# Kernel optimization log

Hardware: AMD Instinct MI355X
Metric: run time of the kernel (lower is better)

The kernel has to match this reference:

```python
import jax, jax.numpy as jnp
import numpy as np

K = 3  # kernel_size from init_kwargs


def setup_inputs() -> dict:
    key = jax.random.key(0)
    x = jax.random.normal(key, (32, 64, 56, 56), dtype=jnp.float32)
    return {"x": x}


def reference(x):
    # Faithful translation of Shift.forward: for each channel i, for each
    # (dy, dx) in the kernel window, emit the padded slice
    # x_pad[:, i, dy:dy+h, dx:dx+w]. Concatenation order is channel-major,
    # then row-major over (dy, dx), which equals stacking the k*k shifts on
    # a new axis right after the channel axis and flattening.
    n, c, h, w = x.shape
    pad = K // 2
    xp = jnp.pad(x, ((0, 0), (0, 0), (pad, pad), (pad, pad)))
    # k*k shifted views of shape [n, c, h, w]; loop is over a small fixed
    # offset set (9 for k=3), not over data dims.
    shifts = jnp.stack(
        [xp[:, :, dy:dy + h, dx:dx + w] for dy in range(K) for dx in range(K)],
        axis=2,
    )  # [n, c, k*k, h, w]
    return shifts.reshape(n, c * K * K, h, w)
```

## Files before the change

kernel.cpp:

```cpp
#include <hip/hip_runtime.h>


#define N_ 32
#define C_ 64
#define H_ 56
#define W_ 56
#define W4 14
#define PLANE (H_ * W_)
#define POS_PER_PLANE (H_ * W4)
#define TOTAL (N_ * C_ * POS_PER_PLANE)

typedef float f4 __attribute__((ext_vector_type(4)));

__global__ __launch_bounds__(256) void shift_kernel(const float* __restrict__ x,
                                                    float* __restrict__ out) {
    int t = blockIdx.x * blockDim.x + threadIdx.x;
    if (t >= TOTAL) return;

    int w4 = t % W4;
    int r  = t / W4;
    int h  = r % H_;
    int nc = r / H_;

    int w0 = w4 * 4;
    const float* plane = x + (long)nc * PLANE;

    float rowbuf[3][6];
#pragma unroll
    for (int d = 0; d < 3; ++d) {
        int ih = h + d - 1;
        if (ih < 0 || ih >= H_) {
#pragma unroll
            for (int j = 0; j < 6; ++j) rowbuf[d][j] = 0.f;
        } else {
            const float* rp = plane + ih * W_;
            f4 v = *(const f4*)(rp + w0);
            rowbuf[d][1] = v.x;
            rowbuf[d][2] = v.y;
            rowbuf[d][3] = v.z;
            rowbuf[d][4] = v.w;
            rowbuf[d][0] = (w4 > 0)      ? rp[w0 - 1] : 0.f;
            rowbuf[d][5] = (w4 < W4 - 1) ? rp[w0 + 4] : 0.f;
        }
    }

    float* ob = out + ((long)(nc * 9) * H_ + h) * W_ + w0;
#pragma unroll
    for (int dy = 0; dy < 3; ++dy) {
#pragma unroll
        for (int dx = 0; dx < 3; ++dx) {
            f4 v = { rowbuf[dy][dx],     rowbuf[dy][dx + 1],
                     rowbuf[dy][dx + 2], rowbuf[dy][dx + 3] };
            *(f4*)(ob + (long)(dy * 3 + dx) * PLANE) = v;
        }
    }
}

extern "C" void kernel_launch(void* const* d_in, const int* in_sizes, int n_in,
                              void* d_out, int out_size, void* d_ws, size_t ws_size,
                              hipStream_t stream) {
    const float* x = (const float*)d_in[0];
    float* out = (float*)d_out;

    int block = 256;
    int grid = (TOTAL + block - 1) / block;
    shift_kernel<<<grid, block, 0, stream>>>(x, out);
}
```

Before: 245.7 us.

## Stage each channel plane in LDS with zero halo and stream shifted outputs

Each block now handles one (n,c) plane. It loads the plane into a zero-padded LDS tile, then writes all nine shifted output planes from LDS using nontemporal vector stores. This replaces redundant, partly unaligned global reads and per-element boundary branches with LDS reads. In exchange it adds two block barriers, an LDS zero-fill pass and unaligned LDS reads, and launches only 2048 blocks.

```diff
diff --git a/kernel.cpp b/kernel.cpp
--- a/kernel.cpp
+++ b/kernel.cpp
@@ -7,51 +7,43 @@
 #define W_ 56
 #define W4 14
 #define PLANE (H_ * W_)
-#define POS_PER_PLANE (H_ * W4)
-#define TOTAL (N_ * C_ * POS_PER_PLANE)
+#define PLANE4 (H_ * W4)
+#define LROW 68
+#define LROWS 58
+#define LSIZE (LROWS * LROW)
 
 typedef float f4 __attribute__((ext_vector_type(4)));
 
 __global__ __launch_bounds__(256) void shift_kernel(const float* __restrict__ x,
-                                                    float* __restrict__ out) {
-    int t = blockIdx.x * blockDim.x + threadIdx.x;
-    if (t >= TOTAL) return;
+                                                    f4* __restrict__ out) {
+    __shared__ float lds[LSIZE];
+    const int tid = threadIdx.x;
+    const int nc  = blockIdx.x;
 
-    int w4 = t % W4;
-    int r  = t / W4;
-    int h  = r % H_;
-    int nc = r / H_;
+    for (int i = tid; i < LSIZE; i += 256) lds[i] = 0.f;
+    __syncthreads();
 
-    int w0 = w4 * 4;
-    const float* plane = x + (long)nc * PLANE;
+    const f4* src = (const f4*)(x + (long)nc * PLANE);
+    for (int i = tid; i < PLANE4; i += 256) {
+        int h  = i / W4;
+        int w4 = i % W4;
+        f4 v = src[i];
+        *(f4*)&lds[(h + 1) * LROW + 4 + 4 * w4] = v;
+    }
+    __syncthreads();
 
-    float rowbuf[3][6];
+    f4* ob = out + (long)nc * 9 * PLANE4;
 #pragma unroll
-    for (int d = 0; d < 3; ++d) {
-        int ih = h + d - 1;
-        if (ih < 0 || ih >= H_) {
-#pragma unroll
-            for (int j = 0; j < 6; ++j) rowbuf[d][j] = 0.f;
-        } else {
-            const float* rp = plane + ih * W_;
-            f4 v = *(const f4*)(rp + w0);
-            rowbuf[d][1] = v.x;
-            rowbuf[d][2] = v.y;
-            rowbuf[d][3] = v.z;
-            rowbuf[d][4] = v.w;
-            rowbuf[d][0] = (w4 > 0)      ? rp[w0 - 1] : 0.f;
-            rowbuf[d][5] = (w4 < W4 - 1) ? rp[w0 + 4] : 0.f;
-        }
-    }
-
-    float* ob = out + ((long)(nc * 9) * H_ + h) * W_ + w0;
-#pragma unroll
-    for (int dy = 0; dy < 3; ++dy) {
-#pragma unroll
-        for (int dx = 0; dx < 3; ++dx) {
-            f4 v = { rowbuf[dy][dx],     rowbuf[dy][dx + 1],
-                     rowbuf[dy][dx + 2], rowbuf[dy][dx + 3] };
-            *(f4*)(ob + (long)(dy * 3 + dx) * PLANE) = v;
+    for (int s = 0; s < 9; ++s) {
+        const int dyi = s / 3;
+        const int dxi = s % 3;
+        f4* op = ob + (long)s * PLANE4;
+        for (int i = tid; i < PLANE4; i += 256) {
+            int h  = i / W4;
+            int w0 = 4 * (i % W4);
+            const float* p = &lds[(h + dyi) * LROW + 3 + dxi + w0];
+            f4 v = { p[0], p[1], p[2], p[3] };
+            __builtin_nontemporal_store(v, op + i);
         }
     }
 }
@@ -60,9 +52,6 @@
                               void* d_out, int out_size, void* d_ws, size_t ws_size,
                               hipStream_t stream) {
     const float* x = (const float*)d_in[0];
-    float* out = (float*)d_out;
-
-    int block = 256;
-    int grid = (TOTAL + block - 1) / block;
-    shift_kernel<<<grid, block, 0, stream>>>(x, out);
+    f4* out = (f4*)d_out;
+    shift_kernel<<<N_ * C_, 256, 0, stream>>>(x, out);
 }
```

Measured after the change: 246.2 us. No clear change (+0.2%).
